# Kernel optimization log

Hardware: AMD Instinct MI355X
Metric: run time of the kernel (lower is better)

## Reference

```python
import jax, jax.numpy as jnp
import numpy as np

HEADS = 6
PS = 7  # window size
DN = ('NCHW', 'OIHW', 'NCHW')


def _conv1x1(x, w):
    return jax.lax.conv_general_dilated(x, w, (1, 1), 'VALID', dimension_numbers=DN)


def _dwconv3(x, w, groups):
    return jax.lax.conv_general_dilated(x, w, (1, 1), 'SAME', dimension_numbers=DN,
                                        feature_group_count=groups)


def _l2norm(t, eps=1e-12):
    # matches torch F.normalize(dim=-1): x / max(||x||_2, eps)
    n = jnp.sqrt(jnp.sum(t * t, axis=-1, keepdims=True))
    return t / jnp.maximum(n, eps)


def setup_inputs() -> dict:
    key = jax.random.key(0)
    k1, k2, k3, k4 = jax.random.split(key, 4)
    B, C, H, W = 2, 180, 448, 448
    x = jax.random.normal(k1, (B, C, H, W), dtype=jnp.float32)
    temperature = jnp.ones((HEADS, 1, 1), dtype=jnp.float32)
    w_qkv = jax.random.normal(k2, (3 * C, C, 1, 1), dtype=jnp.float32) * 0.05
    w_dw = jax.random.normal(k3, (3 * C, 1, 3, 3), dtype=jnp.float32) * 0.05
    w_proj = jax.random.normal(k4, (C, C, 1, 1), dtype=jnp.float32) * 0.05
    return {'x': x, 'temperature': temperature, 'w_qkv': w_qkv, 'w_dw': w_dw, 'w_proj': w_proj}


def reference(x, temperature, w_qkv, w_dw, w_proj):
    b, c, H, W = x.shape
    d = c // HEADS
    hh, ww = H // PS, W // PS

    qkv = _dwconv3(_conv1x1(x, w_qkv), w_dw, 3 * c)  # [b, 3c, H, W]
    q, k, v = jnp.split(qkv, 3, axis=1)

    def rearr(t):
        # 'b (head d) (h ph) (w pw) -> b (h w) head d (ph pw)'
        t = t.reshape(b, HEADS, d, hh, PS, ww, PS)
        t = t.transpose(0, 3, 5, 1, 2, 4, 6)  # b, hh, ww, head, d, ph, pw
        return t.reshape(b, hh * ww, HEADS, d, PS * PS)

    q, k, v = rearr(q), rearr(k), rearr(v)
    q = _l2norm(q)
    k = _l2norm(k)

    # channel-channel attention per window: [b, n_win, head, d, d]
    attn = jnp.einsum('bnhdp,bnhep->bnhde', q, k) * temperature
    attn = jax.nn.softmax(attn, axis=-1)
    out = jnp.einsum('bnhde,bnhep->bnhdp', attn, v)

    # inverse rearrange: 'b (h w) head d (ph pw) -> b (head d) (h ph) (w pw)'
    out = out.reshape(b, hh, ww, HEADS, d, PS, PS)
    out = out.transpose(0, 3, 4, 1, 5, 2, 6).reshape(b, c, H, W)
    return _conv1x1(out, w_proj)
```

## Files before the change

kernel.cpp:

```cpp
#include <hip/hip_runtime.h>

#define HW 200704
#define WIMG 448
#define VPLANE 229376

typedef __attribute__((ext_vector_type(4))) unsigned int u32x4;
typedef __attribute__((ext_vector_type(4))) float f32x4;
typedef __attribute__((ext_vector_type(8))) short s16x8;

static __device__ __forceinline__ unsigned short f2bf(float f) {
    union { float f; unsigned int u; } v; v.f = f;
    unsigned int u = v.u;
    unsigned int r = u + 0x7FFFu + ((u >> 16) & 1u);
    return (unsigned short)(r >> 16);
}
static __device__ __forceinline__ float bf2f(unsigned short s) {
    union { unsigned int u; float f; } v; v.u = ((unsigned int)s) << 16;
    return v.f;
}

__global__ __launch_bounds__(256) void transpose_cast_kernel(
    const float* __restrict__ x, unsigned short* __restrict__ xT)
{
    const int p0 = blockIdx.x * 64;
    const int tid = threadIdx.x;
    const int pl = tid & 63;

    __shared__ float T[180 * 65];

    for (int ic = tid >> 6; ic < 180; ic += 4)
        T[ic * 65 + pl] = x[(size_t)ic * HW + p0 + pl];
    __syncthreads();

    const int cg = tid >> 6;
    unsigned short* drow = xT + ((size_t)p0 + pl) * 192;
#pragma unroll
    for (int i = 0; i < 6; ++i) {
        int k0 = (cg * 6 + i) * 8;
        unsigned short u[8];
#pragma unroll
        for (int e = 0; e < 8; ++e)
            u[e] = (k0 + e < 180) ? f2bf(T[(k0 + e) * 65 + pl]) : (unsigned short)0;
        *(u32x4*)(drow + k0) = *(const u32x4*)u;
    }
}

__global__ __launch_bounds__(256) void gemm_qkv_kernel(
    const unsigned short* __restrict__ xT, const float* __restrict__ wq,
    unsigned short* __restrict__ A)
{
    const int d    = blockIdx.x;
    const int orig = (d & 7) * 882 + (d >> 3);
    const int pt   = orig / 9;
    const int ocb  = (orig - pt * 9) * 64;
    const int pix0 = pt * 256;
    const int tid  = threadIdx.x;
    const int l    = tid & 63;
    const int w    = tid >> 6;
    const int r15  = l & 15;
    const int g4   = l >> 4;

    __shared__ __align__(16) unsigned short wlds[64 * 200];
    __shared__ __align__(16) unsigned short xs[256 * 40];

    for (int idx = tid; idx < 64 * 24; idx += 256) {
        int row = idx / 24, ch = idx - (idx / 24) * 24;
        int oc = ocb + row;
        unsigned short u[8];
#pragma unroll
        for (int e = 0; e < 8; ++e) {
            int k = ch * 8 + e;
            u[e] = (oc < 540 && k < 180) ? f2bf(wq[oc * 180 + k]) : (unsigned short)0;
        }
        *(u32x4*)(wlds + row * 200 + ch * 8) = *(const u32x4*)u;
    }

    const unsigned short* srow[4];
#pragma unroll
    for (int i = 0; i < 4; ++i)
        srow[i] = xT + ((size_t)pix0 + i * 64 + (tid >> 2)) * 192 + (tid & 3) * 8;
    const int sdst = (tid >> 2) * 40 + (tid & 3) * 8;

    f32x4 acc[4][4];
#pragma unroll
    for (int mi = 0; mi < 4; ++mi)
#pragma unroll
        for (int nt = 0; nt < 4; ++nt) acc[mi][nt] = (f32x4){0.f, 0.f, 0.f, 0.f};

    for (int ks = 0; ks < 6; ++ks) {
        __syncthreads();
#pragma unroll
        for (int i = 0; i < 4; ++i)
            *(u32x4*)(xs + sdst + i * 64 * 40) = *(const u32x4*)(srow[i] + ks * 32);
        __syncthreads();

        s16x8 aW[4], bX[4];
#pragma unroll
        for (int mi = 0; mi < 4; ++mi)
            aW[mi] = __builtin_bit_cast(s16x8,
                     *(const u32x4*)(wlds + (mi * 16 + r15) * 200 + ks * 32 + g4 * 8));
#pragma unroll
        for (int nt = 0; nt < 4; ++nt)
            bX[nt] = __builtin_bit_cast(s16x8,
                     *(const u32x4*)(xs + (w * 64 + nt * 16 + r15) * 40 + g4 * 8));
#pragma unroll
        for (int mi = 0; mi < 4; ++mi)
#pragma unroll
            for (int nt = 0; nt < 4; ++nt)
                acc[mi][nt] = __builtin_amdgcn_mfma_f32_16x16x32_bf16(
                    aW[mi], bX[nt], acc[mi][nt], 0, 0, 0);
    }

#pragma unroll
    for (int mi = 0; mi < 4; ++mi) {
#pragma unroll
        for (int reg = 0; reg < 4; ++reg) {
            int oc = ocb + mi * 16 + g4 * 4 + reg;
            if (oc < 540) {
                unsigned short* orow = A + (size_t)oc * HW + pix0 + w * 64;
#pragma unroll
                for (int nt = 0; nt < 4; ++nt)
                    orow[nt * 16 + r15] = f2bf(acc[mi][nt][reg]);
            }
        }
    }
}

__global__ __launch_bounds__(256) void dw_kernel(
    const unsigned short* __restrict__ A, const float* __restrict__ wdw,
    unsigned short* __restrict__ Bw)
{
    const int wrow = blockIdx.x;
    const int c    = blockIdx.y;
    const int tid  = threadIdx.x;

    const int part = c / 180;
    const int rem  = c - part * 180;
    const int head = rem / 30;
    const int dc   = rem - head * 30;

    __shared__ float Ls[9 * 452];

    float w9[9];
#pragma unroll
    for (int i = 0; i < 9; ++i) w9[i] = wdw[c * 9 + i];

    const int y0 = wrow * 7;
    const unsigned int* Ac32 = (const unsigned int*)(A + (size_t)c * HW);
    for (int idx = tid; idx < 2016; idx += 256) {
        int r  = idx / 224;
        int c2 = idx - r * 224;
        int y  = y0 + r - 1;
        unsigned int v = ((unsigned)y < 448u) ? Ac32[y * 224 + c2] : 0u;
        Ls[r * 452 + 1 + 2 * c2] = bf2f((unsigned short)(v & 0xffffu));
        Ls[r * 452 + 2 + 2 * c2] = bf2f((unsigned short)(v >> 16));
    }
    if (tid < 18) {
        int r = tid >> 1;
        Ls[r * 452 + ((tid & 1) ? 449 : 0)] = 0.f;
    }
    __syncthreads();

    unsigned int* dst = (unsigned int*)(Bw +
        ((size_t)(head * 3 + part) * 30 + dc) * VPLANE + (size_t)wrow * 64 * 56);
#pragma unroll
    for (int k = 0; k < 7; ++k) {
        int o2 = k * 256 + tid;
        int wo = o2 / 28;
        int r2 = o2 - wo * 28;
        unsigned short r2v[2];
#pragma unroll
        for (int e = 0; e < 2; ++e) {
            int rm = r2 * 2 + e;
            float acc = 0.f;
            if (rm < 49) {
                int ph = rm / 7, pw = rm - ph * 7;
                int xb = wo * 7 + pw;
                const float* L = Ls + ph * 452 + xb;
                acc = w9[0]*L[0] + w9[1]*L[1] + w9[2]*L[2];
                L += 452;
                acc += w9[3]*L[0] + w9[4]*L[1] + w9[5]*L[2];
                L += 452;
                acc += w9[6]*L[0] + w9[7]*L[1] + w9[8]*L[2];
            }
            r2v[e] = (rm < 49) ? f2bf(acc) : (unsigned short)0;
        }
        dst[o2] = (unsigned int)r2v[0] | ((unsigned int)r2v[1] << 16);
    }
}

__global__ __launch_bounds__(256) void attn2_kernel(
    const unsigned short* __restrict__ Bw,
    const float* __restrict__ temperature,
    unsigned short* __restrict__ Cwt)
{
    __shared__ __align__(16) unsigned short lds[4][6144];
    __shared__ float invs[4][64];

    const int w    = threadIdx.x >> 6;
    const int l    = threadIdx.x & 63;
    const int wg   = blockIdx.x;
    const int head = blockIdx.y;
    const int win  = wg * 4 + w;
    const float temp = temperature[head];
    unsigned short* U = lds[w];
    float* inv = invs[w];
    const int r15 = l & 15;
    const int g4  = l >> 4;

    {
        const unsigned short* plane0 =
            Bw + (size_t)(head * 3) * 30 * VPLANE + (size_t)win * 56;
#pragma unroll
        for (int i = 0; i < 8; ++i) {
            int part = i >> 2;
            int row  = ((i & 3) << 3) | (l >> 3);
            int c    = l & 7;
            u32x4 v = {0u, 0u, 0u, 0u};
            if (row < 30 && c < 7)
                v = *(const u32x4*)(plane0 + (size_t)(part * 30 + row) * VPLANE + c * 8);
            *(u32x4*)(U + part * 2048 + row * 64 + ((c ^ (row & 7)) << 3)) = v;
        }
    }
    {
        const unsigned short* vplane =
            Bw + (size_t)(head * 3 + 2) * 30 * VPLANE + (size_t)win * 56;
        for (int j = 0; j < 23; ++j) {
            int idx = j * 64 + l;
            if (idx < 1470) {
                int dc = idx / 49;
                int p  = idx - dc * 49;
                unsigned short val = vplane[(size_t)dc * VPLANE + p];
                int col = (((dc >> 3) ^ (p & 3)) << 3) | (dc & 7);
                U[4096 + p * 32 + col] = val;
            }
        }
        int c30 = ((3 ^ (l & 3)) << 3) | 6;
        U[4096 + l * 32 + c30]     = 0;
        U[4096 + l * 32 + c30 + 1] = 0;
    }
    __syncthreads();

    s16x8 aQ[2][2], bK[2][2];
#pragma unroll
    for (int mi = 0; mi < 2; ++mi)
#pragma unroll
        for (int kk = 0; kk < 2; ++kk) {
            int r  = mi * 16 + r15;
            int gk = kk * 4 + g4;
            int so = ((gk ^ (r & 7)) << 3);
            aQ[mi][kk] = __builtin_bit_cast(s16x8, *(const u32x4*)(U + r * 64 + so));
            bK[mi][kk] = __builtin_bit_cast(s16x8, *(const u32x4*)(U + 2048 + r * 64 + so));
        }

    f32x4 s[2][2], dq[2], dk[2];
#pragma unroll
    for (int mi = 0; mi < 2; ++mi) {
        dq[mi] = (f32x4){0.f, 0.f, 0.f, 0.f};
        dk[mi] = (f32x4){0.f, 0.f, 0.f, 0.f};
#pragma unroll
        for (int nj = 0; nj < 2; ++nj) s[mi][nj] = (f32x4){0.f, 0.f, 0.f, 0.f};
    }

#pragma unroll
    for (int kk = 0; kk < 2; ++kk) {
#pragma unroll
        for (int mi = 0; mi < 2; ++mi) {
#pragma unroll
            for (int nj = 0; nj < 2; ++nj)
                s[mi][nj] = __builtin_amdgcn_mfma_f32_16x16x32_bf16(
                    aQ[mi][kk], bK[nj][kk], s[mi][nj], 0, 0, 0);
            dq[mi] = __builtin_amdgcn_mfma_f32_16x16x32_bf16(
                aQ[mi][kk], aQ[mi][kk], dq[mi], 0, 0, 0);
            dk[mi] = __builtin_amdgcn_mfma_f32_16x16x32_bf16(
                bK[mi][kk], bK[mi][kk], dk[mi], 0, 0, 0);
        }
    }

#pragma unroll
    for (int mi = 0; mi < 2; ++mi)
#pragma unroll
        for (int reg = 0; reg < 4; ++reg) {
            int row = g4 * 4 + reg;
            if (row == r15) {
                inv[mi * 16 + row]      = 1.f / fmaxf(sqrtf(dq[mi][reg]), 1e-12f);
                inv[32 + mi * 16 + row] = 1.f / fmaxf(sqrtf(dk[mi][reg]), 1e-12f);
            }
        }
    __syncthreads();

    float pr[2][2][4];
    float cinvk0 = inv[32 + r15];
    float cinvk1 = inv[32 + 16 + r15];
#pragma unroll
    for (int mi = 0; mi < 2; ++mi)
#pragma unroll
        for (int reg = 0; reg < 4; ++reg) {
            float qi = inv[mi * 16 + g4 * 4 + reg];
            float v0 = s[mi][0][reg] * qi * cinvk0 * temp;
            float v1 = s[mi][1][reg] * qi * cinvk1 * temp;
            if (16 + r15 >= 30) v1 = -1e30f;
            float m = fmaxf(v0, v1);
#pragma unroll
            for (int off = 1; off < 16; off <<= 1) m = fmaxf(m, __shfl_xor(m, off));
            float e0 = __expf(v0 - m);
            float e1 = __expf(v1 - m);
            float sum = e0 + e1;
#pragma unroll
            for (int off = 1; off < 16; off <<= 1) sum += __shfl_xor(sum, off);
            float rs = 1.f / sum;
            pr[mi][0][reg] = e0 * rs;
            pr[mi][1][reg] = e1 * rs;
        }

#pragma unroll
    for (int mi = 0; mi < 2; ++mi)
#pragma unroll
        for (int nj = 0; nj < 2; ++nj)
#pragma unroll
            for (int reg = 0; reg < 4; ++reg) {
                int row = mi * 16 + g4 * 4 + reg;
                int col = nj * 16 + r15;
                int scol = (((col >> 3) ^ (row & 3)) << 3) | (col & 7);
                U[row * 32 + scol] = f2bf(pr[mi][nj][reg]);
            }
    __syncthreads();

    s16x8 aP[2], bV[4];
#pragma unroll
    for (int mi = 0; mi < 2; ++mi) {
        int i = mi * 16 + r15;
        aP[mi] = __builtin_bit_cast(s16x8,
                 *(const u32x4*)(U + i * 32 + ((g4 ^ (i & 3)) << 3)));
    }
#pragma unroll
    for (int nt = 0; nt < 4; ++nt) {
        int p = nt * 16 + r15;
        bV[nt] = __builtin_bit_cast(s16x8,
                 *(const u32x4*)(U + 4096 + p * 32 + ((g4 ^ (p & 3)) << 3)));
    }
    f32x4 o[2][4];
#pragma unroll
    for (int mi = 0; mi < 2; ++mi)
#pragma unroll
        for (int nt = 0; nt < 4; ++nt) {
            o[mi][nt] = (f32x4){0.f, 0.f, 0.f, 0.f};
            o[mi][nt] = __builtin_amdgcn_mfma_f32_16x16x32_bf16(
                aP[mi], bV[nt], o[mi][nt], 0, 0, 0);
        }

    unsigned short* dst = Cwt + ((size_t)win * 49) * 192 + head * 30;
#pragma unroll
    for (int mi = 0; mi < 2; ++mi) {
        int ch0 = mi * 16 + g4 * 4;
#pragma unroll
        for (int nt = 0; nt < 4; ++nt) {
            int p = nt * 16 + r15;
            if (p < 49) {
                unsigned int lo = (unsigned int)f2bf(o[mi][nt][0]) |
                                  ((unsigned int)f2bf(o[mi][nt][1]) << 16);
                *(unsigned int*)(dst + (size_t)p * 192 + ch0) = lo;
                if (ch0 + 2 < 30) {
                    unsigned int hi = (unsigned int)f2bf(o[mi][nt][2]) |
                                      ((unsigned int)f2bf(o[mi][nt][3]) << 16);
                    *(unsigned int*)(dst + (size_t)p * 192 + ch0 + 2) = hi;
                }
            }
        }
    }
    if (head == 5 && g4 == 0) {
        unsigned short* zrow = Cwt + ((size_t)win * 49) * 192 + 180;
#pragma unroll
        for (int nt = 0; nt < 4; ++nt) {
            int p = nt * 16 + r15;
            if (p < 49) {
                *(unsigned int*)(zrow + (size_t)p * 192 + 0) = 0u;
                *(unsigned int*)(zrow + (size_t)p * 192 + 2) = 0u;
                *(unsigned int*)(zrow + (size_t)p * 192 + 4) = 0u;
            }
        }
    }
}

__global__ __launch_bounds__(256) void gemm_proj_kernel(
    const unsigned short* __restrict__ Cwt, const float* __restrict__ wp,
    float* __restrict__ out)
{
    const int d    = blockIdx.x;
    const int orig = (d & 7) * 294 + (d >> 3);
    const int pt   = orig / 3;
    const int ocb  = (orig - pt * 3) * 64;
    const int pix0 = pt * 256;
    const int tid  = threadIdx.x;
    const int l    = tid & 63;
    const int w    = tid >> 6;
    const int r15  = l & 15;
    const int g4   = l >> 4;

    __shared__ __align__(16) unsigned short wlds[64 * 200];
    __shared__ __align__(16) unsigned short xs[256 * 40];

    for (int idx = tid; idx < 64 * 24; idx += 256) {
        int row = idx / 24, ch = idx - (idx / 24) * 24;
        int oc = ocb + row;
        unsigned short u[8];
#pragma unroll
        for (int e = 0; e < 8; ++e) {
            int k = ch * 8 + e;
            u[e] = (oc < 180 && k < 180) ? f2bf(wp[oc * 180 + k]) : (unsigned short)0;
        }
        *(u32x4*)(wlds + row * 200 + ch * 8) = *(const u32x4*)u;
    }

    const unsigned short* srow[4];
#pragma unroll
    for (int i = 0; i < 4; ++i) {
        int P = pix0 + i * 64 + (tid >> 2);
        int win = P / 49, p = P - win * 49;
        srow[i] = Cwt + ((size_t)win * 49 + p) * 192 + (tid & 3) * 8;
    }
    const int sdst = (tid >> 2) * 40 + (tid & 3) * 8;

    f32x4 acc[4][4];
#pragma unroll
    for (int mi = 0; mi < 4; ++mi)
#pragma unroll
        for (int nt = 0; nt < 4; ++nt) acc[mi][nt] = (f32x4){0.f, 0.f, 0.f, 0.f};

    for (int ks = 0; ks < 6; ++ks) {
        __syncthreads();
#pragma unroll
        for (int i = 0; i < 4; ++i)
            *(u32x4*)(xs + sdst + i * 64 * 40) = *(const u32x4*)(srow[i] + ks * 32);
        __syncthreads();

        s16x8 aW[4], bX[4];
#pragma unroll
        for (int mi = 0; mi < 4; ++mi)
            aW[mi] = __builtin_bit_cast(s16x8,
                     *(const u32x4*)(wlds + (mi * 16 + r15) * 200 + ks * 32 + g4 * 8));
#pragma unroll
        for (int nt = 0; nt < 4; ++nt)
            bX[nt] = __builtin_bit_cast(s16x8,
                     *(const u32x4*)(xs + (w * 64 + nt * 16 + r15) * 40 + g4 * 8));
#pragma unroll
        for (int mi = 0; mi < 4; ++mi)
#pragma unroll
            for (int nt = 0; nt < 4; ++nt)
                acc[mi][nt] = __builtin_amdgcn_mfma_f32_16x16x32_bf16(
                    aW[mi], bX[nt], acc[mi][nt], 0, 0, 0);
    }

    int poff[4];
#pragma unroll
    for (int nt = 0; nt < 4; ++nt) {
        int P = pix0 + w * 64 + nt * 16 + r15;
        int win = P / 49, p = P - win * 49;
        int ph = p / 7, pw2 = p - ph * 7;
        poff[nt] = ((win >> 6) * 7 + ph) * WIMG + (win & 63) * 7 + pw2;
    }
#pragma unroll
    for (int mi = 0; mi < 4; ++mi) {
#pragma unroll
        for (int reg = 0; reg < 4; ++reg) {
            int oc = ocb + mi * 16 + g4 * 4 + reg;
            if (oc < 180) {
#pragma unroll
                for (int nt = 0; nt < 4; ++nt)
                    out[(size_t)oc * HW + poff[nt]] = acc[mi][nt][reg];
            }
        }
    }
}

extern "C" void kernel_launch(void* const* d_in, const int* in_sizes, int n_in,
                              void* d_out, int out_size, void* d_ws, size_t ws_size,
                              hipStream_t stream) {
    const float* x           = (const float*)d_in[0];
    const float* temperature = (const float*)d_in[1];
    const float* w_qkv       = (const float*)d_in[2];
    const float* w_dw        = (const float*)d_in[3];
    const float* w_proj      = (const float*)d_in[4];
    float* out = (float*)d_out;

    if (ws_size < 618627072ull) return;
    unsigned short* xT  = (unsigned short*)d_ws;
    unsigned short* A   = (unsigned short*)((char*)d_ws + 77070336ull);
    unsigned short* Bw  = (unsigned short*)((char*)d_ws + 293830656ull);
    unsigned short* Cwt = (unsigned short*)((char*)d_ws + 541556736ull);

    for (int b = 0; b < 2; ++b) {
        const float* xb = x + (size_t)b * 180 * HW;
        float* ob = out + (size_t)b * 180 * HW;
        transpose_cast_kernel<<<dim3(HW / 64), 256, 0, stream>>>(xb, xT);
        gemm_qkv_kernel<<<dim3(7056), 256, 0, stream>>>(xT, w_qkv, A);
        dw_kernel<<<dim3(64, 540), 256, 0, stream>>>(A, w_dw, Bw);
        attn2_kernel<<<dim3(1024, 6), 256, 0, stream>>>(Bw, temperature, Cwt);
        gemm_proj_kernel<<<dim3(2352), 256, 0, stream>>>(Cwt, w_proj, ob);
    }
}
```

Measured before the change: 1.349 ms.

## Double-buffer QKV GEMM activations via direct global-to-LDS loads with XOR swizzle

The QKV projection GEMM now uses 512-thread blocks covering 128 output channels instead of 64, so each staged activation tile is reused by twice as many channels. Activation tiles are loaded straight into LDS with global_load_lds into two buffers in 64-wide K chunks, so the next chunk's load overlaps the current chunk's MFMAs. An XOR swizzle on the LDS layout is meant to avoid bank conflicts. In exchange, the block uses more LDS and has more threads, which lowers occupancy, and the last of the 5 channel tiles is partly idle because 540 is not a multiple of 128.

```diff
diff --git a/kernel.cpp b/kernel.cpp
--- a/kernel.cpp
+++ b/kernel.cpp
@@ -45,25 +45,28 @@
     }
 }
 
-__global__ __launch_bounds__(256) void gemm_qkv_kernel(
+__global__ __launch_bounds__(512) void gemm_qkv_kernel(
     const unsigned short* __restrict__ xT, const float* __restrict__ wq,
     unsigned short* __restrict__ A)
 {
     const int d    = blockIdx.x;
-    const int orig = (d & 7) * 882 + (d >> 3);
-    const int pt   = orig / 9;
-    const int ocb  = (orig - pt * 9) * 64;
+    const int orig = (d & 7) * 490 + (d >> 3);
+    const int pt   = orig / 5;
+    const int oct  = orig - pt * 5;
+    const int ocb  = oct * 128;
     const int pix0 = pt * 256;
     const int tid  = threadIdx.x;
     const int l    = tid & 63;
     const int w    = tid >> 6;
     const int r15  = l & 15;
     const int g4   = l >> 4;
-
-    __shared__ __align__(16) unsigned short wlds[64 * 200];
-    __shared__ __align__(16) unsigned short xs[256 * 40];
-
-    for (int idx = tid; idx < 64 * 24; idx += 256) {
+    const int q    = w & 3;
+    const int mh   = w >> 2;
+
+    __shared__ __align__(16) unsigned short wlds[128 * 200];
+    __shared__ __align__(16) unsigned short xs[2][256 * 64];
+
+    for (int idx = tid; idx < 128 * 24; idx += 512) {
         int row = idx / 24, ch = idx - (idx / 24) * 24;
         int oc = ocb + row;
         unsigned short u[8];
@@ -75,11 +78,20 @@
         *(u32x4*)(wlds + row * 200 + ch * 8) = *(const u32x4*)u;
     }
 
-    const unsigned short* srow[4];
-#pragma unroll
-    for (int i = 0; i < 4; ++i)
-        srow[i] = xT + ((size_t)pix0 + i * 64 + (tid >> 2)) * 192 + (tid & 3) * 8;
-    const int sdst = (tid >> 2) * 40 + (tid & 3) * 8;
+    auto stage = [&](int c, int buf) {
+#pragma unroll
+        for (int i = 0; i < 4; ++i) {
+            int slot = i * 512 + tid;
+            int px   = slot >> 3;
+            int g    = slot & 7;
+            const unsigned short* src =
+                xT + ((size_t)pix0 + px) * 192 + c * 64 + ((g ^ (px & 7)) << 3);
+            __builtin_amdgcn_global_load_lds(
+                (const __attribute__((address_space(1))) unsigned int*)(const void*)src,
+                (__attribute__((address_space(3))) unsigned int*)(void*)(&xs[buf][slot * 8]),
+                16, 0, 0);
+        }
+    };
 
     f32x4 acc[4][4];
 #pragma unroll
@@ -87,37 +99,42 @@
 #pragma unroll
         for (int nt = 0; nt < 4; ++nt) acc[mi][nt] = (f32x4){0.f, 0.f, 0.f, 0.f};
 
-    for (int ks = 0; ks < 6; ++ks) {
+    stage(0, 0);
+    __syncthreads();
+
+    for (int c = 0; c < 3; ++c) {
+        if (c < 2) stage(c + 1, (c + 1) & 1);
+        const unsigned short* xb = xs[c & 1];
+#pragma unroll
+        for (int kk = 0; kk < 2; ++kk) {
+            s16x8 aW[4], bX[4];
+#pragma unroll
+            for (int mi = 0; mi < 4; ++mi)
+                aW[mi] = __builtin_bit_cast(s16x8, *(const u32x4*)(
+                    wlds + (mh * 64 + mi * 16 + r15) * 200 + c * 64 + kk * 32 + g4 * 8));
+#pragma unroll
+            for (int nt = 0; nt < 4; ++nt) {
+                int px = q * 64 + nt * 16 + r15;
+                bX[nt] = __builtin_bit_cast(s16x8, *(const u32x4*)(
+                    xb + px * 64 + (((kk * 4 + g4) ^ (px & 7)) << 3)));
+            }
+#pragma unroll
+            for (int mi = 0; mi < 4; ++mi)
+#pragma unroll
+                for (int nt = 0; nt < 4; ++nt)
+                    acc[mi][nt] = __builtin_amdgcn_mfma_f32_16x16x32_bf16(
+                        aW[mi], bX[nt], acc[mi][nt], 0, 0, 0);
+        }
         __syncthreads();
-#pragma unroll
-        for (int i = 0; i < 4; ++i)
-            *(u32x4*)(xs + sdst + i * 64 * 40) = *(const u32x4*)(srow[i] + ks * 32);
-        __syncthreads();
-
-        s16x8 aW[4], bX[4];
-#pragma unroll
-        for (int mi = 0; mi < 4; ++mi)
-            aW[mi] = __builtin_bit_cast(s16x8,
-                     *(const u32x4*)(wlds + (mi * 16 + r15) * 200 + ks * 32 + g4 * 8));
-#pragma unroll
-        for (int nt = 0; nt < 4; ++nt)
-            bX[nt] = __builtin_bit_cast(s16x8,
-                     *(const u32x4*)(xs + (w * 64 + nt * 16 + r15) * 40 + g4 * 8));
-#pragma unroll
-        for (int mi = 0; mi < 4; ++mi)
-#pragma unroll
-            for (int nt = 0; nt < 4; ++nt)
-                acc[mi][nt] = __builtin_amdgcn_mfma_f32_16x16x32_bf16(
-                    aW[mi], bX[nt], acc[mi][nt], 0, 0, 0);
     }
 
 #pragma unroll
     for (int mi = 0; mi < 4; ++mi) {
 #pragma unroll
         for (int reg = 0; reg < 4; ++reg) {
-            int oc = ocb + mi * 16 + g4 * 4 + reg;
+            int oc = ocb + mh * 64 + mi * 16 + g4 * 4 + reg;
             if (oc < 540) {
-                unsigned short* orow = A + (size_t)oc * HW + pix0 + w * 64;
+                unsigned short* orow = A + (size_t)oc * HW + pix0 + q * 64;
 #pragma unroll
                 for (int nt = 0; nt < 4; ++nt)
                     orow[nt * 16 + r15] = f2bf(acc[mi][nt][reg]);
@@ -493,7 +510,7 @@
         const float* xb = x + (size_t)b * 180 * HW;
         float* ob = out + (size_t)b * 180 * HW;
         transpose_cast_kernel<<<dim3(HW / 64), 256, 0, stream>>>(xb, xT);
-        gemm_qkv_kernel<<<dim3(7056), 256, 0, stream>>>(xT, w_qkv, A);
+        gemm_qkv_kernel<<<dim3(3920), 512, 0, stream>>>(xT, w_qkv, A);
         dw_kernel<<<dim3(64, 540), 256, 0, stream>>>(A, w_dw, Bw);
         attn2_kernel<<<dim3(1024, 6), 256, 0, stream>>>(Bw, temperature, Cwt);
         gemm_proj_kernel<<<dim3(2352), 256, 0, stream>>>(Cwt, w_proj, ob);
```

New measurement: 1.376 ms. 1.02x slower.
